# Kernel tuning notes

Measured on AMD Instinct MI355X. Metric: run time of the kernel, lower is better.

The kernel has to match this reference:

```python
import jax, jax.numpy as jnp
import numpy as np

B, S, D = 2, 2048, 1024
H = 16
HD = D // H  # 64
SCALE = HD ** -0.5


def setup_inputs() -> dict:
    key = jax.random.key(0)
    ks = jax.random.split(key, 9)
    init = lambda k, shape: jax.random.normal(k, shape, dtype=jnp.float32) * (1.0 / np.sqrt(shape[-1]))
    return {
        "x": jax.random.normal(ks[0], (B, S, D), dtype=jnp.float32),
        "wq": init(ks[1], (D, D)), "bq": jnp.zeros((D,), jnp.float32),
        "wk": init(ks[2], (D, D)), "bk": jnp.zeros((D,), jnp.float32),
        "wv": init(ks[3], (D, D)), "bv": jnp.zeros((D,), jnp.float32),
        "wo": init(ks[4], (D, D)), "bo": jnp.zeros((D,), jnp.float32),
    }


def reference(x, wq, bq, wk, bk, wv, bv, wo, bo):
    b, s, d = x.shape
    # projections -> [b, h, s, hd]
    q = (x @ wq + bq).reshape(b, s, H, HD).transpose(0, 2, 1, 3)
    k = (x @ wk + bk).reshape(b, s, H, HD).transpose(0, 2, 1, 3)
    v = (x @ wv + bv).reshape(b, s, H, HD).transpose(0, 2, 1, 3)
    # full causal attention (chunked loop in original computes exactly this)
    scores = jnp.einsum("bhqd,bhkd->bhqk", q, k) * SCALE
    causal = jnp.tril(jnp.ones((s, s), dtype=bool))
    scores = jnp.where(causal, scores, -jnp.inf)
    weights = jax.nn.softmax(scores, axis=-1)
    out = jnp.einsum("bhqk,bhkd->bhqd", weights, v)
    out = out.transpose(0, 2, 1, 3).reshape(b, s, d)
    return out @ wo + bo
```

## Files before the change

### kernel.cpp

```cpp
#include <hip/hip_runtime.h>
#include <hip/hip_bf16.h>
#include <cstdint>

#define B_  2
#define S_  2048
#define D_  1024
#define H_  16
#define HD_ 64
#define M_  (B_ * S_)
static constexpr float SC_LOG2E = 0.125f * 1.44269504088896f;

typedef __bf16 bf16x8 __attribute__((ext_vector_type(8)));
typedef __bf16 bf16x4 __attribute__((ext_vector_type(4)));
typedef float  f32x4  __attribute__((ext_vector_type(4)));

#define PPLANE (256 * 2 * 512)

__device__ __forceinline__ unsigned short f2b(float f) {
  union { float f; unsigned u; } x; x.f = f;
  unsigned r = x.u + 0x7FFF + ((x.u >> 16) & 1);
  return (unsigned short)(r >> 16);
}

__device__ __forceinline__ void gl_lds16(const unsigned short* g, unsigned short* l) {
  __builtin_amdgcn_global_load_lds((const __attribute__((address_space(1))) void*)g,
                                   (__attribute__((address_space(3))) void*)l, 16, 0, 0);
}

__device__ __forceinline__ void bar_lgkm() {
  asm volatile("s_waitcnt lgkmcnt(0)\n\ts_barrier" ::: "memory");
}
__device__ __forceinline__ void bar_vm2() {
  asm volatile("s_waitcnt vmcnt(2) lgkmcnt(0)\n\ts_barrier" ::: "memory");
}
__device__ __forceinline__ void bar_vm0() {
  asm volatile("s_waitcnt vmcnt(0) lgkmcnt(0)\n\ts_barrier" ::: "memory");
}

__global__ void cvt_all_kernel(const float* __restrict__ x,
                               const float* __restrict__ w0, const float* __restrict__ w1,
                               const float* __restrict__ w2, const float* __restrict__ w3,
                               unsigned short* __restrict__ xb,
                               unsigned short* __restrict__ o0, unsigned short* __restrict__ o1,
                               unsigned short* __restrict__ o2, unsigned short* __restrict__ o3) {
  int tx = threadIdx.x, ty = threadIdx.y;
  if (blockIdx.z == 4) {
    int tid = ty * 32 + tx;
    int base = ((int)blockIdx.y * 32 + (int)blockIdx.x) * 1024 + tid;
    const float4* xf = (const float4*)x;
    ushort4* ob = (ushort4*)xb;
#pragma unroll
    for (int j = 0; j < 4; j++) {
      float4 v = xf[base + j * 256];
      ushort4 r;
      r.x = f2b(v.x); r.y = f2b(v.y); r.z = f2b(v.z); r.w = f2b(v.w);
      ob[base + j * 256] = r;
    }
    return;
  }
  const float* w = blockIdx.z == 0 ? w0 : blockIdx.z == 1 ? w1 : blockIdx.z == 2 ? w2 : w3;
  unsigned short* o = blockIdx.z == 0 ? o0 : blockIdx.z == 1 ? o1 : blockIdx.z == 2 ? o2 : o3;
  __shared__ float t[32][33];
  int x0 = blockIdx.x * 32, y0 = blockIdx.y * 32;
#pragma unroll
  for (int j = 0; j < 4; j++)
    t[ty + j * 8][tx] = w[(size_t)(y0 + ty + j * 8) * D_ + x0 + tx];
  __syncthreads();
#pragma unroll
  for (int j = 0; j < 4; j++)
    o[(size_t)(x0 + ty + j * 8) * D_ + y0 + tx] = f2b(t[tx][ty + j * 8]);
}

__global__ __launch_bounds__(512) void qkv_gemm_kernel(
    const unsigned short* __restrict__ xb,
    const unsigned short* __restrict__ wqt, const unsigned short* __restrict__ wkt,
    const unsigned short* __restrict__ wvt,
    const float* __restrict__ bq, const float* __restrict__ bk, const float* __restrict__ bv,
    unsigned short* __restrict__ qo, unsigned short* __restrict__ ko, unsigned short* __restrict__ vo) {
  const unsigned short* wt = blockIdx.z == 0 ? wqt : blockIdx.z == 1 ? wkt : wvt;
  const float* bias        = blockIdx.z == 0 ? bq  : blockIdx.z == 1 ? bk  : bv;
  unsigned short* out      = blockIdx.z == 0 ? qo  : blockIdx.z == 1 ? ko  : vo;
  const float scl = blockIdx.z == 0 ? SC_LOG2E : 1.0f;

  __shared__ __align__(16) unsigned short smem[6 * 4096];
  const int tid = threadIdx.x;
  const int lane = tid & 63, wid = tid >> 6;
  const int wm = wid & 1, wn = wid >> 1;
  const int m0 = blockIdx.x * 128, n0 = blockIdx.y * 128;
  const int l15 = lane & 15, q4 = lane >> 4;
  const int srow = tid >> 2, skc = (tid & 3) * 8;

  f32x4 zero = {0.f, 0.f, 0.f, 0.f};
  f32x4 acc[4][2];
#pragma unroll
  for (int mt = 0; mt < 4; mt++)
#pragma unroll
    for (int nt = 0; nt < 2; nt++) acc[mt][nt] = zero;

  const unsigned short* ap = xb + (size_t)(m0 + srow) * D_ + skc;
  const unsigned short* bp = wt + (size_t)(n0 + srow) * D_ + skc;
  gl_lds16(ap,      smem + tid * 8);
  gl_lds16(bp,      smem + 12288 + tid * 8);
  gl_lds16(ap + 32, smem + 4096 + tid * 8);
  gl_lds16(bp + 32, smem + 12288 + 4096 + tid * 8);

  int bc = 0;
  for (int it = 0; it < 32; it++) {
    if (it < 31) bar_vm2(); else bar_vm0();
    if (it + 2 < 32) {
      int bn_ = bc < 1 ? bc + 2 : bc - 1;
      gl_lds16(ap + (it + 2) * 32, smem + bn_ * 4096 + tid * 8);
      gl_lds16(bp + (it + 2) * 32, smem + 12288 + bn_ * 4096 + tid * 8);
    }
    const unsigned short* Ab = smem + bc * 4096;
    const unsigned short* Bb = smem + 12288 + bc * 4096;
    bf16x8 af[4], bfv[2];
#pragma unroll
    for (int mt = 0; mt < 4; mt++) af[mt]  = *(const bf16x8*)(Ab + (wm * 64 + mt * 16 + l15) * 32 + q4 * 8);
#pragma unroll
    for (int nt = 0; nt < 2; nt++) bfv[nt] = *(const bf16x8*)(Bb + (wn * 32 + nt * 16 + l15) * 32 + q4 * 8);
#pragma unroll
    for (int mt = 0; mt < 4; mt++)
#pragma unroll
      for (int nt = 0; nt < 2; nt++)
        acc[mt][nt] = __builtin_amdgcn_mfma_f32_16x16x32_bf16(af[mt], bfv[nt], acc[mt][nt], 0, 0, 0);
    bc = bc == 2 ? 0 : bc + 1;
  }

  if (blockIdx.z < 2) {
#pragma unroll
    for (int nt = 0; nt < 2; nt++) {
      int n = n0 + wn * 32 + nt * 16 + l15;
      float bn = bias[n];
      int h = n >> 6, hd = n & 63;
#pragma unroll
      for (int mt = 0; mt < 4; mt++) {
#pragma unroll
        for (int r = 0; r < 4; r++) {
          int m = m0 + wm * 64 + mt * 16 + q4 * 4 + r;
          int b = m >> 11, s = m & (S_ - 1);
          out[(((size_t)(b * H_ + h)) * S_ + s) * HD_ + hd] = f2b((acc[mt][nt][r] + bn) * scl);
        }
      }
    }
  } else {
    unsigned short* buf = smem;
#pragma unroll
    for (int p = 0; p < 2; p++) {
      __syncthreads();
      if ((wn >> 1) == p) {
#pragma unroll
        for (int nt = 0; nt < 2; nt++) {
          int np = (wn & 1) * 32 + nt * 16 + l15;
          float bn = bias[n0 + p * 64 + np];
#pragma unroll
          for (int mt = 0; mt < 4; mt++) {
            f32x4 vb = acc[mt][nt];
            vb[0] += bn; vb[1] += bn; vb[2] += bn; vb[3] += bn;
            bf16x4 pk = __builtin_convertvector(vb, bf16x4);
            *(bf16x4*)(&buf[np * 136 + wm * 64 + mt * 16 + q4 * 4]) = pk;
          }
        }
      }
      __syncthreads();
#pragma unroll
      for (int i = 0; i < 2; i++) {
        int ci = tid + i * 512;
        int np = ci >> 4, c = ci & 15;
        int n = n0 + p * 64 + np;
        int h = n >> 6, hd = n & 63;
        int m = m0 + c * 8;
        int b = m >> 11, s = m & (S_ - 1);
        *(uint4*)(out + (((size_t)(b * H_ + h)) * HD_ + hd) * S_ + s) = *(const uint4*)(buf + np * 136 + c * 8);
      }
    }
  }
}

__global__ __launch_bounds__(512, 6) void attn_kernel(
    const unsigned short* __restrict__ Q, const unsigned short* __restrict__ K,
    const unsigned short* __restrict__ Vt_g, unsigned short* __restrict__ O,
    float* __restrict__ part) {
  const int id = blockIdx.x;
  const int g = id & 255, r = id >> 8;
  const int bh = g & 31, j = g >> 5;
  const bool heavy = (r < 2);
  const int qi = heavy ? (15 - j) : j;
  const int split = heavy ? r : 0;
  const int b = bh >> 4, h = bh & 15;
  const unsigned short* Qh = Q    + (size_t)bh * S_ * HD_;
  const unsigned short* Kh = K    + (size_t)bh * S_ * HD_;
  const unsigned short* Vh = Vt_g + (size_t)bh * HD_ * S_;

  __shared__ __align__(16) unsigned short Ks[2][64 * 64];
  __shared__ __align__(16) unsigned short Vt[2][64 * 64];
  __shared__ __align__(16) unsigned short Ps[8][16 * 72];

  const int tid = threadIdx.x, lane = tid & 63, w = tid >> 6;
  const int l15 = lane & 15, q4 = lane >> 4;
  const int kx = (l15 & 7) << 3;
  const int kcA = (q4 * 8) ^ kx, kcB = (q4 * 8 + 32) ^ kx;
  const int vc0 = (q4 * 8) ^ kx, vc1 = (32 + q4 * 8) ^ kx;
  unsigned short* Pw = &Ps[w][0];

  const int srow = tid >> 3;
  const int scolS = (((tid & 7) ^ (srow & 7)) * 8);
  const unsigned short* kg = Kh + (size_t)srow * HD_ + (tid & 7) * 8;
  const unsigned short* vg = Vh + (size_t)srow * S_  + (tid & 7) * 8;

  const int q0 = qi * 128;
  const int nst = heavy ? (qi + 1) : (2 * qi + 2);
  const int kstep = heavy ? 2 : 1;
  const int qlo = q0 + w * 16;
  const int qmax = qlo + 15;
  const int qrow = qlo + l15;

  const unsigned short* qp = Qh + (size_t)qrow * HD_ + q4 * 8;
  bf16x8 bq0 = *(const bf16x8*)(qp);
  bf16x8 bq1 = *(const bf16x8*)(qp + 32);

  float m_i = -1e30f, l_i = 0.f;
  f32x4 zero = {0.f, 0.f, 0.f, 0.f};
  f32x4 o_acc[4];
#pragma unroll
  for (int t4 = 0; t4 < 4; t4++) o_acc[t4] = zero;

  uint4 kp = *(const uint4*)(kg + (size_t)split * 64 * HD_);
  uint4 vp = *(const uint4*)(vg + split * 64);

  for (int s = 0; s < nst; s++) {
    const int kt = kstep * s + split;
    const int k0 = kt * 64;
    unsigned short* Kb = Ks[s & 1];
    unsigned short* Vb = Vt[s & 1];
    *(uint4*)(Kb + srow * 64 + scolS) = kp;
    *(uint4*)(Vb + srow * 64 + scolS) = vp;
    bar_lgkm();
    if (s + 1 < nst) {
      const int ktn = kt + kstep;
      kp = *(const uint4*)(kg + (size_t)ktn * 64 * HD_);
      vp = *(const uint4*)(vg + ktn * 64);
    }

    if (k0 <= qmax) {
      f32x4 sc[4];
#pragma unroll
      for (int nt = 0; nt < 4; nt++) sc[nt] = zero;
      __builtin_amdgcn_s_setprio(1);
#pragma unroll
      for (int nt = 0; nt < 4; nt++) {
        bf16x8 ak0 = *(const bf16x8*)(Kb + (nt * 16 + l15) * 64 + kcA);
        bf16x8 ak1 = *(const bf16x8*)(Kb + (nt * 16 + l15) * 64 + kcB);
        sc[nt] = __builtin_amdgcn_mfma_f32_16x16x32_bf16(ak0, bq0, sc[nt], 0, 0, 0);
        sc[nt] = __builtin_amdgcn_mfma_f32_16x16x32_bf16(ak1, bq1, sc[nt], 0, 0, 0);
      }
      __builtin_amdgcn_s_setprio(0);

      if ((k0 + 63) > qlo) {
#pragma unroll
        for (int nt = 0; nt < 4; nt++)
#pragma unroll
          for (int r2 = 0; r2 < 4; r2++) {
            int key = k0 + nt * 16 + q4 * 4 + r2;
            if (key > qrow) sc[nt][r2] = -1e30f;
          }
      }

      float am[4];
#pragma unroll
      for (int nt = 0; nt < 4; nt++)
        am[nt] = fmaxf(fmaxf(sc[nt][0], sc[nt][1]), fmaxf(sc[nt][2], sc[nt][3]));
      am[0] = fmaxf(am[0], am[2]); am[1] = fmaxf(am[1], am[3]);
      float mx = fmaxf(am[0], am[1]);
      mx = fmaxf(mx, __shfl_xor(mx, 16));
      mx = fmaxf(mx, __shfl_xor(mx, 32));
      mx = fmaxf(mx, m_i);

      if (!__all(mx - m_i <= 10.0f)) {
        float alpha = __builtin_amdgcn_exp2f(m_i - mx);
        m_i = mx;
        l_i *= alpha;
#pragma unroll
        for (int r2 = 0; r2 < 4; r2++) {
          float ar = __shfl(alpha, q4 * 4 + r2);
          o_acc[0][r2] *= ar; o_acc[1][r2] *= ar; o_acc[2][r2] *= ar; o_acc[3][r2] *= ar;
        }
      }

      float sm[4];
#pragma unroll
      for (int nt = 0; nt < 4; nt++) {
        f32x4 pv;
#pragma unroll
        for (int r2 = 0; r2 < 4; r2++) pv[r2] = __builtin_amdgcn_exp2f(sc[nt][r2] - m_i);
        sc[nt] = pv;
        sm[nt] = (pv[0] + pv[1]) + (pv[2] + pv[3]);
      }
      float rs = (sm[0] + sm[2]) + (sm[1] + sm[3]);
      rs += __shfl_xor(rs, 16);
      rs += __shfl_xor(rs, 32);
      l_i += rs;

#pragma unroll
      for (int nt = 0; nt < 4; nt++) {
        bf16x4 pk = __builtin_convertvector(sc[nt], bf16x4);
        *(bf16x4*)(Pw + l15 * 72 + nt * 16 + q4 * 4) = pk;
      }
      __threadfence_block();
      bf16x8 ap0 = *(const bf16x8*)(Pw + l15 * 72 + q4 * 8);
      bf16x8 ap1 = *(const bf16x8*)(Pw + l15 * 72 + 32 + q4 * 8);
      __builtin_amdgcn_s_setprio(1);
#pragma unroll
      for (int nt2 = 0; nt2 < 4; nt2++) {
        bf16x8 bv0 = *(const bf16x8*)(Vb + (nt2 * 16 + l15) * 64 + vc0);
        o_acc[nt2] = __builtin_amdgcn_mfma_f32_16x16x32_bf16(ap0, bv0, o_acc[nt2], 0, 0, 0);
      }
#pragma unroll
      for (int nt2 = 0; nt2 < 4; nt2++) {
        bf16x8 bv1 = *(const bf16x8*)(Vb + (nt2 * 16 + l15) * 64 + vc1);
        o_acc[nt2] = __builtin_amdgcn_mfma_f32_16x16x32_bf16(ap1, bv1, o_acc[nt2], 0, 0, 0);
      }
      __builtin_amdgcn_s_setprio(0);
    }
  }

  if (heavy) {
    float* P = part + ((size_t)(g * 2 + split) * 512 + tid);
#pragma unroll
    for (int nt2 = 0; nt2 < 4; nt2++)
#pragma unroll
      for (int r2 = 0; r2 < 4; r2++) P[(size_t)(nt2 * 4 + r2) * PPLANE] = o_acc[nt2][r2];
    P[(size_t)16 * PPLANE] = m_i;
    P[(size_t)17 * PPLANE] = l_i;
  } else {
#pragma unroll
    for (int r2 = 0; r2 < 4; r2++) {
      float lr = __shfl(l_i, q4 * 4 + r2);
      float inv = 1.0f / lr;
      int s_ = q0 + w * 16 + q4 * 4 + r2;
#pragma unroll
      for (int nt2 = 0; nt2 < 4; nt2++)
        O[((size_t)(b * S_ + s_)) * D_ + h * HD_ + nt2 * 16 + l15] = f2b(o_acc[nt2][r2] * inv);
    }
  }
}

__global__ __launch_bounds__(512) void attn_merge_kernel(
    const float* __restrict__ part, unsigned short* __restrict__ O) {
  const int g = blockIdx.x;
  const int bh = g & 31, j = g >> 5;
  const int qi = 15 - j;
  const int b = bh >> 4, h = bh & 15;
  const int tid = threadIdx.x, lane = tid & 63, w = tid >> 6;
  const int l15 = lane & 15, q4 = lane >> 4;

  const float* P0 = part + ((size_t)(g * 2 + 0) * 512 + tid);
  const float* P1 = part + ((size_t)(g * 2 + 1) * 512 + tid);
  float o0[16], o1[16];
#pragma unroll
  for (int i = 0; i < 16; i++) {
    o0[i] = P0[(size_t)i * PPLANE];
    o1[i] = P1[(size_t)i * PPLANE];
  }
  float m0 = P0[(size_t)16 * PPLANE], l0 = P0[(size_t)17 * PPLANE];
  float m1 = P1[(size_t)16 * PPLANE], l1 = P1[(size_t)17 * PPLANE];
  float m  = fmaxf(m0, m1);
  float a0 = __builtin_amdgcn_exp2f(m0 - m);
  float a1 = __builtin_amdgcn_exp2f(m1 - m);
  float l  = l0 * a0 + l1 * a1;

  const int q0 = qi * 128;
#pragma unroll
  for (int r2 = 0; r2 < 4; r2++) {
    float ar0 = __shfl(a0, q4 * 4 + r2);
    float ar1 = __shfl(a1, q4 * 4 + r2);
    float inv = 1.0f / __shfl(l, q4 * 4 + r2);
    int s_ = q0 + w * 16 + q4 * 4 + r2;
#pragma unroll
    for (int nt2 = 0; nt2 < 4; nt2++)
      O[((size_t)(b * S_ + s_)) * D_ + h * HD_ + nt2 * 16 + l15] =
          f2b((o0[nt2 * 4 + r2] * ar0 + o1[nt2 * 4 + r2] * ar1) * inv);
  }
}

__global__ __launch_bounds__(512) void out_gemm_kernel(
    const unsigned short* __restrict__ ab, const unsigned short* __restrict__ wot,
    const float* __restrict__ bo, float* __restrict__ out) {
  __shared__ __align__(16) unsigned short smem[6 * 4096];
  const int tid = threadIdx.x;
  const int lane = tid & 63, wid = tid >> 6;
  const int wm = wid & 1, wn = wid >> 1;
  const int m0 = blockIdx.x * 128, n0 = blockIdx.y * 128;
  const int l15 = lane & 15, q4 = lane >> 4;
  const int srow = tid >> 2, skc = (tid & 3) * 8;

  f32x4 zero = {0.f, 0.f, 0.f, 0.f};
  f32x4 acc[4][2];
#pragma unroll
  for (int mt = 0; mt < 4; mt++)
#pragma unroll
    for (int nt = 0; nt < 2; nt++) acc[mt][nt] = zero;

  const unsigned short* ap = ab  + (size_t)(m0 + srow) * D_ + skc;
  const unsigned short* bp = wot + (size_t)(n0 + srow) * D_ + skc;
  gl_lds16(ap,      smem + tid * 8);
  gl_lds16(bp,      smem + 12288 + tid * 8);
  gl_lds16(ap + 32, smem + 4096 + tid * 8);
  gl_lds16(bp + 32, smem + 12288 + 4096 + tid * 8);

  int bc = 0;
  for (int it = 0; it < 32; it++) {
    if (it < 31) bar_vm2(); else bar_vm0();
    if (it + 2 < 32) {
      int bn_ = bc < 1 ? bc + 2 : bc - 1;
      gl_lds16(ap + (it + 2) * 32, smem + bn_ * 4096 + tid * 8);
      gl_lds16(bp + (it + 2) * 32, smem + 12288 + bn_ * 4096 + tid * 8);
    }
    const unsigned short* Ab = smem + bc * 4096;
    const unsigned short* Bb = smem + 12288 + bc * 4096;
    bf16x8 af[4], bfv[2];
#pragma unroll
    for (int mt = 0; mt < 4; mt++) af[mt]  = *(const bf16x8*)(Ab + (wm * 64 + mt * 16 + l15) * 32 + q4 * 8);
#pragma unroll
    for (int nt = 0; nt < 2; nt++) bfv[nt] = *(const bf16x8*)(Bb + (wn * 32 + nt * 16 + l15) * 32 + q4 * 8);
#pragma unroll
    for (int mt = 0; mt < 4; mt++)
#pragma unroll
      for (int nt = 0; nt < 2; nt++)
        acc[mt][nt] = __builtin_amdgcn_mfma_f32_16x16x32_bf16(af[mt], bfv[nt], acc[mt][nt], 0, 0, 0);
    bc = bc == 2 ? 0 : bc + 1;
  }

#pragma unroll
  for (int nt = 0; nt < 2; nt++) {
    int n = n0 + wn * 32 + nt * 16 + l15;
    float bn = bo[n];
#pragma unroll
    for (int mt = 0; mt < 4; mt++) {
#pragma unroll
      for (int r = 0; r < 4; r++) {
        int m = m0 + wm * 64 + mt * 16 + q4 * 4 + r;
        out[(size_t)m * D_ + n] = acc[mt][nt][r] + bn;
      }
    }
  }
}

extern "C" void kernel_launch(void* const* d_in, const int* in_sizes, int n_in,
                              void* d_out, int out_size, void* d_ws, size_t ws_size,
                              hipStream_t stream) {
  const float* x  = (const float*)d_in[0];
  const float* wq = (const float*)d_in[1];
  const float* bq = (const float*)d_in[2];
  const float* wk = (const float*)d_in[3];
  const float* bk = (const float*)d_in[4];
  const float* wv = (const float*)d_in[5];
  const float* bv = (const float*)d_in[6];
  const float* wo = (const float*)d_in[7];
  const float* bo = (const float*)d_in[8];
  float* out = (float*)d_out;

  char* ws = (char*)d_ws;
  unsigned short* xb  = (unsigned short*)(ws);
  unsigned short* wqt = (unsigned short*)(ws + (8u  << 20));
  unsigned short* wkt = (unsigned short*)(ws + (10u << 20));
  unsigned short* wvt = (unsigned short*)(ws + (12u << 20));
  unsigned short* wot = (unsigned short*)(ws + (14u << 20));
  unsigned short* qb  = (unsigned short*)(ws + (16u << 20));
  unsigned short* kb  = (unsigned short*)(ws + (24u << 20));
  unsigned short* vtg = (unsigned short*)(ws + (32u << 20));
  float*          prt = (float*)(ws + (40u << 20));
  unsigned short* ab  = xb;

  cvt_all_kernel<<<dim3(32, 32, 5), dim3(32, 8), 0, stream>>>(x, wq, wk, wv, wo, xb, wqt, wkt, wvt, wot);
  qkv_gemm_kernel<<<dim3(32, 8, 3), dim3(512), 0, stream>>>(xb, wqt, wkt, wvt, bq, bk, bv, qb, kb, vtg);
  attn_kernel<<<dim3(768), dim3(512), 0, stream>>>(qb, kb, vtg, ab, prt);
  attn_merge_kernel<<<dim3(256), dim3(512), 0, stream>>>(prt, ab);
  out_gemm_kernel<<<dim3(32, 8), dim3(512), 0, stream>>>(ab, wot, bo, out);
}
```

Baseline: 181.5 us.

## Give each attention wave 32 query rows and halve block size to 256 threads

Each wave now processes two 16-row query groups against the same K/V tiles, so the K fragments loaded from LDS are reused across twice as many MFMAs. The block shrinks to 4 waves, each thread stages two K/V chunks, and the partial-result layout and merge kernel are rewritten for the new 256-thread mapping. This roughly doubles accumulator and score registers per wave and lowers the occupancy hint. Causal masking also becomes coarser per wave, which may waste some work on diagonal tiles.

```diff
diff --git a/kernel.cpp b/kernel.cpp
--- a/kernel.cpp
+++ b/kernel.cpp
@@ -14,7 +14,7 @@
 typedef __bf16 bf16x4 __attribute__((ext_vector_type(4)));
 typedef float  f32x4  __attribute__((ext_vector_type(4)));
 
-#define PPLANE (256 * 2 * 512)
+#define PPL2 (256 * 2 * 256)
 
 __device__ __forceinline__ unsigned short f2b(float f) {
   union { float f; unsigned u; } x; x.f = f;
@@ -177,7 +177,7 @@
   }
 }
 
-__global__ __launch_bounds__(512, 6) void attn_kernel(
+__global__ __launch_bounds__(256, 3) void attn_kernel(
     const unsigned short* __restrict__ Q, const unsigned short* __restrict__ K,
     const unsigned short* __restrict__ Vt_g, unsigned short* __restrict__ O,
     float* __restrict__ part) {
@@ -194,7 +194,7 @@
 
   __shared__ __align__(16) unsigned short Ks[2][64 * 64];
   __shared__ __align__(16) unsigned short Vt[2][64 * 64];
-  __shared__ __align__(16) unsigned short Ps[8][16 * 72];
+  __shared__ __align__(16) unsigned short Ps[4][32 * 72];
 
   const int tid = threadIdx.x, lane = tid & 63, w = tid >> 6;
   const int l15 = lane & 15, q4 = lane >> 4;
@@ -203,149 +203,188 @@
   const int vc0 = (q4 * 8) ^ kx, vc1 = (32 + q4 * 8) ^ kx;
   unsigned short* Pw = &Ps[w][0];
 
-  const int srow = tid >> 3;
-  const int scolS = (((tid & 7) ^ (srow & 7)) * 8);
-  const unsigned short* kg = Kh + (size_t)srow * HD_ + (tid & 7) * 8;
-  const unsigned short* vg = Vh + (size_t)srow * S_  + (tid & 7) * 8;
+  int soff[2], kgo[2], vgo[2];
+#pragma unroll
+  for (int jj = 0; jj < 2; jj++) {
+    int c = tid + jj * 256, row = c >> 3, c8 = c & 7;
+    soff[jj] = row * 64 + ((c8 ^ (row & 7)) * 8);
+    kgo[jj] = row * HD_ + c8 * 8;
+    vgo[jj] = row * S_  + c8 * 8;
+  }
 
   const int q0 = qi * 128;
   const int nst = heavy ? (qi + 1) : (2 * qi + 2);
   const int kstep = heavy ? 2 : 1;
-  const int qlo = q0 + w * 16;
-  const int qmax = qlo + 15;
-  const int qrow = qlo + l15;
-
-  const unsigned short* qp = Qh + (size_t)qrow * HD_ + q4 * 8;
-  bf16x8 bq0 = *(const bf16x8*)(qp);
-  bf16x8 bq1 = *(const bf16x8*)(qp + 32);
-
-  float m_i = -1e30f, l_i = 0.f;
+  const int qlo = q0 + w * 32;
+  const int qmax = qlo + 31;
+
+  bf16x8 bq[2][2];
+#pragma unroll
+  for (int grp = 0; grp < 2; grp++) {
+    const unsigned short* qp = Qh + (size_t)(qlo + grp * 16 + l15) * HD_ + q4 * 8;
+    bq[grp][0] = *(const bf16x8*)(qp);
+    bq[grp][1] = *(const bf16x8*)(qp + 32);
+  }
+
+  float m_i[2] = {-1e30f, -1e30f}, l_i[2] = {0.f, 0.f};
   f32x4 zero = {0.f, 0.f, 0.f, 0.f};
-  f32x4 o_acc[4];
-#pragma unroll
-  for (int t4 = 0; t4 < 4; t4++) o_acc[t4] = zero;
-
-  uint4 kp = *(const uint4*)(kg + (size_t)split * 64 * HD_);
-  uint4 vp = *(const uint4*)(vg + split * 64);
+  f32x4 o_acc[2][4];
+#pragma unroll
+  for (int grp = 0; grp < 2; grp++)
+#pragma unroll
+    for (int t4 = 0; t4 < 4; t4++) o_acc[grp][t4] = zero;
+
+  uint4 kp[2], vp[2];
+#pragma unroll
+  for (int jj = 0; jj < 2; jj++) {
+    kp[jj] = *(const uint4*)(Kh + (size_t)split * 64 * HD_ + kgo[jj]);
+    vp[jj] = *(const uint4*)(Vh + split * 64 + vgo[jj]);
+  }
 
   for (int s = 0; s < nst; s++) {
     const int kt = kstep * s + split;
     const int k0 = kt * 64;
     unsigned short* Kb = Ks[s & 1];
     unsigned short* Vb = Vt[s & 1];
-    *(uint4*)(Kb + srow * 64 + scolS) = kp;
-    *(uint4*)(Vb + srow * 64 + scolS) = vp;
+#pragma unroll
+    for (int jj = 0; jj < 2; jj++) {
+      *(uint4*)(Kb + soff[jj]) = kp[jj];
+      *(uint4*)(Vb + soff[jj]) = vp[jj];
+    }
     bar_lgkm();
     if (s + 1 < nst) {
       const int ktn = kt + kstep;
-      kp = *(const uint4*)(kg + (size_t)ktn * 64 * HD_);
-      vp = *(const uint4*)(vg + ktn * 64);
+#pragma unroll
+      for (int jj = 0; jj < 2; jj++) {
+        kp[jj] = *(const uint4*)(Kh + (size_t)ktn * 64 * HD_ + kgo[jj]);
+        vp[jj] = *(const uint4*)(Vh + ktn * 64 + vgo[jj]);
+      }
     }
 
     if (k0 <= qmax) {
-      f32x4 sc[4];
-#pragma unroll
-      for (int nt = 0; nt < 4; nt++) sc[nt] = zero;
+      f32x4 sc[2][4];
+#pragma unroll
+      for (int grp = 0; grp < 2; grp++)
+#pragma unroll
+        for (int nt = 0; nt < 4; nt++) sc[grp][nt] = zero;
       __builtin_amdgcn_s_setprio(1);
 #pragma unroll
       for (int nt = 0; nt < 4; nt++) {
         bf16x8 ak0 = *(const bf16x8*)(Kb + (nt * 16 + l15) * 64 + kcA);
         bf16x8 ak1 = *(const bf16x8*)(Kb + (nt * 16 + l15) * 64 + kcB);
-        sc[nt] = __builtin_amdgcn_mfma_f32_16x16x32_bf16(ak0, bq0, sc[nt], 0, 0, 0);
-        sc[nt] = __builtin_amdgcn_mfma_f32_16x16x32_bf16(ak1, bq1, sc[nt], 0, 0, 0);
+        sc[0][nt] = __builtin_amdgcn_mfma_f32_16x16x32_bf16(ak0, bq[0][0], sc[0][nt], 0, 0, 0);
+        sc[0][nt] = __builtin_amdgcn_mfma_f32_16x16x32_bf16(ak1, bq[0][1], sc[0][nt], 0, 0, 0);
+        sc[1][nt] = __builtin_amdgcn_mfma_f32_16x16x32_bf16(ak0, bq[1][0], sc[1][nt], 0, 0, 0);
+        sc[1][nt] = __builtin_amdgcn_mfma_f32_16x16x32_bf16(ak1, bq[1][1], sc[1][nt], 0, 0, 0);
       }
       __builtin_amdgcn_s_setprio(0);
 
-      if ((k0 + 63) > qlo) {
+#pragma unroll
+      for (int grp = 0; grp < 2; grp++) {
+        const int qg = qlo + grp * 16;
+        const int qrow = qg + l15;
+        if ((k0 + 63) > qg) {
+#pragma unroll
+          for (int nt = 0; nt < 4; nt++)
+#pragma unroll
+            for (int r2 = 0; r2 < 4; r2++) {
+              int key = k0 + nt * 16 + q4 * 4 + r2;
+              if (key > qrow) sc[grp][nt][r2] = -1e30f;
+            }
+        }
+        float am[4];
 #pragma unroll
         for (int nt = 0; nt < 4; nt++)
+          am[nt] = fmaxf(fmaxf(sc[grp][nt][0], sc[grp][nt][1]), fmaxf(sc[grp][nt][2], sc[grp][nt][3]));
+        am[0] = fmaxf(am[0], am[2]); am[1] = fmaxf(am[1], am[3]);
+        float mx = fmaxf(am[0], am[1]);
+        mx = fmaxf(mx, __shfl_xor(mx, 16));
+        mx = fmaxf(mx, __shfl_xor(mx, 32));
+        mx = fmaxf(mx, m_i[grp]);
+
+        if (!__all(mx - m_i[grp] <= 10.0f)) {
+          float alpha = __builtin_amdgcn_exp2f(m_i[grp] - mx);
+          m_i[grp] = mx;
+          l_i[grp] *= alpha;
 #pragma unroll
           for (int r2 = 0; r2 < 4; r2++) {
-            int key = k0 + nt * 16 + q4 * 4 + r2;
-            if (key > qrow) sc[nt][r2] = -1e30f;
+            float ar = __shfl(alpha, q4 * 4 + r2);
+            o_acc[grp][0][r2] *= ar; o_acc[grp][1][r2] *= ar;
+            o_acc[grp][2][r2] *= ar; o_acc[grp][3][r2] *= ar;
           }
-      }
-
-      float am[4];
-#pragma unroll
-      for (int nt = 0; nt < 4; nt++)
-        am[nt] = fmaxf(fmaxf(sc[nt][0], sc[nt][1]), fmaxf(sc[nt][2], sc[nt][3]));
-      am[0] = fmaxf(am[0], am[2]); am[1] = fmaxf(am[1], am[3]);
-      float mx = fmaxf(am[0], am[1]);
-      mx = fmaxf(mx, __shfl_xor(mx, 16));
-      mx = fmaxf(mx, __shfl_xor(mx, 32));
-      mx = fmaxf(mx, m_i);
-
-      if (!__all(mx - m_i <= 10.0f)) {
-        float alpha = __builtin_amdgcn_exp2f(m_i - mx);
-        m_i = mx;
-        l_i *= alpha;
-#pragma unroll
-        for (int r2 = 0; r2 < 4; r2++) {
-          float ar = __shfl(alpha, q4 * 4 + r2);
-          o_acc[0][r2] *= ar; o_acc[1][r2] *= ar; o_acc[2][r2] *= ar; o_acc[3][r2] *= ar;
         }
-      }
-
-      float sm[4];
-#pragma unroll
-      for (int nt = 0; nt < 4; nt++) {
-        f32x4 pv;
-#pragma unroll
-        for (int r2 = 0; r2 < 4; r2++) pv[r2] = __builtin_amdgcn_exp2f(sc[nt][r2] - m_i);
-        sc[nt] = pv;
-        sm[nt] = (pv[0] + pv[1]) + (pv[2] + pv[3]);
-      }
-      float rs = (sm[0] + sm[2]) + (sm[1] + sm[3]);
-      rs += __shfl_xor(rs, 16);
-      rs += __shfl_xor(rs, 32);
-      l_i += rs;
-
-#pragma unroll
-      for (int nt = 0; nt < 4; nt++) {
-        bf16x4 pk = __builtin_convertvector(sc[nt], bf16x4);
-        *(bf16x4*)(Pw + l15 * 72 + nt * 16 + q4 * 4) = pk;
+
+        float sm[4];
+#pragma unroll
+        for (int nt = 0; nt < 4; nt++) {
+          f32x4 pv;
+#pragma unroll
+          for (int r2 = 0; r2 < 4; r2++) pv[r2] = __builtin_amdgcn_exp2f(sc[grp][nt][r2] - m_i[grp]);
+          sc[grp][nt] = pv;
+          sm[nt] = (pv[0] + pv[1]) + (pv[2] + pv[3]);
+        }
+        float rs = (sm[0] + sm[2]) + (sm[1] + sm[3]);
+        rs += __shfl_xor(rs, 16);
+        rs += __shfl_xor(rs, 32);
+        l_i[grp] += rs;
+
+#pragma unroll
+        for (int nt = 0; nt < 4; nt++) {
+          bf16x4 pk = __builtin_convertvector(sc[grp][nt], bf16x4);
+          *(bf16x4*)(Pw + (grp * 16 + l15) * 72 + nt * 16 + q4 * 4) = pk;
+        }
       }
       __threadfence_block();
-      bf16x8 ap0 = *(const bf16x8*)(Pw + l15 * 72 + q4 * 8);
-      bf16x8 ap1 = *(const bf16x8*)(Pw + l15 * 72 + 32 + q4 * 8);
+      bf16x8 a0g0 = *(const bf16x8*)(Pw + l15 * 72 + q4 * 8);
+      bf16x8 a1g0 = *(const bf16x8*)(Pw + l15 * 72 + 32 + q4 * 8);
+      bf16x8 a0g1 = *(const bf16x8*)(Pw + (16 + l15) * 72 + q4 * 8);
+      bf16x8 a1g1 = *(const bf16x8*)(Pw + (16 + l15) * 72 + 32 + q4 * 8);
       __builtin_amdgcn_s_setprio(1);
 #pragma unroll
       for (int nt2 = 0; nt2 < 4; nt2++) {
         bf16x8 bv0 = *(const bf16x8*)(Vb + (nt2 * 16 + l15) * 64 + vc0);
-        o_acc[nt2] = __builtin_amdgcn_mfma_f32_16x16x32_bf16(ap0, bv0, o_acc[nt2], 0, 0, 0);
+        o_acc[0][nt2] = __builtin_amdgcn_mfma_f32_16x16x32_bf16(a0g0, bv0, o_acc[0][nt2], 0, 0, 0);
+        o_acc[1][nt2] = __builtin_amdgcn_mfma_f32_16x16x32_bf16(a0g1, bv0, o_acc[1][nt2], 0, 0, 0);
       }
 #pragma unroll
       for (int nt2 = 0; nt2 < 4; nt2++) {
         bf16x8 bv1 = *(const bf16x8*)(Vb + (nt2 * 16 + l15) * 64 + vc1);
-        o_acc[nt2] = __builtin_amdgcn_mfma_f32_16x16x32_bf16(ap1, bv1, o_acc[nt2], 0, 0, 0);
+        o_acc[0][nt2] = __builtin_amdgcn_mfma_f32_16x16x32_bf16(a1g0, bv1, o_acc[0][nt2], 0, 0, 0);
+        o_acc[1][nt2] = __builtin_amdgcn_mfma_f32_16x16x32_bf16(a1g1, bv1, o_acc[1][nt2], 0, 0, 0);
       }
       __builtin_amdgcn_s_setprio(0);
     }
   }
 
   if (heavy) {
-    float* P = part + ((size_t)(g * 2 + split) * 512 + tid);
-#pragma unroll
-    for (int nt2 = 0; nt2 < 4; nt2++)
-#pragma unroll
-      for (int r2 = 0; r2 < 4; r2++) P[(size_t)(nt2 * 4 + r2) * PPLANE] = o_acc[nt2][r2];
-    P[(size_t)16 * PPLANE] = m_i;
-    P[(size_t)17 * PPLANE] = l_i;
+    float* P = part + ((size_t)(g * 2 + split) * 256 + tid);
+#pragma unroll
+    for (int grp = 0; grp < 2; grp++)
+#pragma unroll
+      for (int nt2 = 0; nt2 < 4; nt2++)
+#pragma unroll
+        for (int r2 = 0; r2 < 4; r2++)
+          P[(size_t)(grp * 16 + nt2 * 4 + r2) * PPL2] = o_acc[grp][nt2][r2];
+    P[(size_t)32 * PPL2] = m_i[0];
+    P[(size_t)33 * PPL2] = m_i[1];
+    P[(size_t)34 * PPL2] = l_i[0];
+    P[(size_t)35 * PPL2] = l_i[1];
   } else {
 #pragma unroll
-    for (int r2 = 0; r2 < 4; r2++) {
-      float lr = __shfl(l_i, q4 * 4 + r2);
-      float inv = 1.0f / lr;
-      int s_ = q0 + w * 16 + q4 * 4 + r2;
-#pragma unroll
-      for (int nt2 = 0; nt2 < 4; nt2++)
-        O[((size_t)(b * S_ + s_)) * D_ + h * HD_ + nt2 * 16 + l15] = f2b(o_acc[nt2][r2] * inv);
-    }
-  }
-}
-
-__global__ __launch_bounds__(512) void attn_merge_kernel(
+    for (int grp = 0; grp < 2; grp++)
+#pragma unroll
+      for (int r2 = 0; r2 < 4; r2++) {
+        float lr = __shfl(l_i[grp], q4 * 4 + r2);
+        float inv = 1.0f / lr;
+        int s_ = qlo + grp * 16 + q4 * 4 + r2;
+#pragma unroll
+        for (int nt2 = 0; nt2 < 4; nt2++)
+          O[((size_t)(b * S_ + s_)) * D_ + h * HD_ + nt2 * 16 + l15] = f2b(o_acc[grp][nt2][r2] * inv);
+      }
+  }
+}
+
+__global__ __launch_bounds__(256) void attn_merge_kernel(
     const float* __restrict__ part, unsigned short* __restrict__ O) {
   const int g = blockIdx.x;
   const int bh = g & 31, j = g >> 5;
@@ -353,33 +392,35 @@
   const int b = bh >> 4, h = bh & 15;
   const int tid = threadIdx.x, lane = tid & 63, w = tid >> 6;
   const int l15 = lane & 15, q4 = lane >> 4;
-
-  const float* P0 = part + ((size_t)(g * 2 + 0) * 512 + tid);
-  const float* P1 = part + ((size_t)(g * 2 + 1) * 512 + tid);
-  float o0[16], o1[16];
-#pragma unroll
-  for (int i = 0; i < 16; i++) {
-    o0[i] = P0[(size_t)i * PPLANE];
-    o1[i] = P1[(size_t)i * PPLANE];
-  }
-  float m0 = P0[(size_t)16 * PPLANE], l0 = P0[(size_t)17 * PPLANE];
-  float m1 = P1[(size_t)16 * PPLANE], l1 = P1[(size_t)17 * PPLANE];
-  float m  = fmaxf(m0, m1);
-  float a0 = __builtin_amdgcn_exp2f(m0 - m);
-  float a1 = __builtin_amdgcn_exp2f(m1 - m);
-  float l  = l0 * a0 + l1 * a1;
-
-  const int q0 = qi * 128;
-#pragma unroll
-  for (int r2 = 0; r2 < 4; r2++) {
-    float ar0 = __shfl(a0, q4 * 4 + r2);
-    float ar1 = __shfl(a1, q4 * 4 + r2);
-    float inv = 1.0f / __shfl(l, q4 * 4 + r2);
-    int s_ = q0 + w * 16 + q4 * 4 + r2;
-#pragma unroll
-    for (int nt2 = 0; nt2 < 4; nt2++)
-      O[((size_t)(b * S_ + s_)) * D_ + h * HD_ + nt2 * 16 + l15] =
-          f2b((o0[nt2 * 4 + r2] * ar0 + o1[nt2 * 4 + r2] * ar1) * inv);
+  const int qlo = qi * 128 + w * 32;
+
+  const float* P0 = part + ((size_t)(g * 2 + 0) * 256 + tid);
+  const float* P1 = part + ((size_t)(g * 2 + 1) * 256 + tid);
+#pragma unroll
+  for (int grp = 0; grp < 2; grp++) {
+    float o0[16], o1[16];
+#pragma unroll
+    for (int i = 0; i < 16; i++) {
+      o0[i] = P0[(size_t)(grp * 16 + i) * PPL2];
+      o1[i] = P1[(size_t)(grp * 16 + i) * PPL2];
+    }
+    float m0 = P0[(size_t)(32 + grp) * PPL2], l0 = P0[(size_t)(34 + grp) * PPL2];
+    float m1 = P1[(size_t)(32 + grp) * PPL2], l1 = P1[(size_t)(34 + grp) * PPL2];
+    float m  = fmaxf(m0, m1);
+    float a0 = __builtin_amdgcn_exp2f(m0 - m);
+    float a1 = __builtin_amdgcn_exp2f(m1 - m);
+    float l  = l0 * a0 + l1 * a1;
+#pragma unroll
+    for (int r2 = 0; r2 < 4; r2++) {
+      float ar0 = __shfl(a0, q4 * 4 + r2);
+      float ar1 = __shfl(a1, q4 * 4 + r2);
+      float inv = 1.0f / __shfl(l, q4 * 4 + r2);
+      int s_ = qlo + grp * 16 + q4 * 4 + r2;
+#pragma unroll
+      for (int nt2 = 0; nt2 < 4; nt2++)
+        O[((size_t)(b * S_ + s_)) * D_ + h * HD_ + nt2 * 16 + l15] =
+            f2b((o0[nt2 * 4 + r2] * ar0 + o1[nt2 * 4 + r2] * ar1) * inv);
+    }
   }
 }
 
@@ -474,7 +515,7 @@
 
   cvt_all_kernel<<<dim3(32, 32, 5), dim3(32, 8), 0, stream>>>(x, wq, wk, wv, wo, xb, wqt, wkt, wvt, wot);
   qkv_gemm_kernel<<<dim3(32, 8, 3), dim3(512), 0, stream>>>(xb, wqt, wkt, wvt, bq, bk, bv, qb, kb, vtg);
-  attn_kernel<<<dim3(768), dim3(512), 0, stream>>>(qb, kb, vtg, ab, prt);
-  attn_merge_kernel<<<dim3(256), dim3(512), 0, stream>>>(prt, ab);
+  attn_kernel<<<dim3(768), dim3(256), 0, stream>>>(qb, kb, vtg, ab, prt);
+  attn_merge_kernel<<<dim3(256), dim3(256), 0, stream>>>(prt, ab);
   out_gemm_kernel<<<dim3(32, 8), dim3(512), 0, stream>>>(ab, wot, bo, out);
 }
```

Result: slower. 199.3 us (+9.8%).

## Fuse split-KV merge into attention via atomic counter, drop merge kernel

Applied to the files above, without the earlier changes.

The separate merge kernel is removed. Each heavy attention block writes its partial output, then increments a per-group atomic counter. The block that arrives second reads the other split's partial from global memory and writes the final normalized output. The counter is zeroed inside the conversion kernel. The P scratch row stride also changes from 72 to 68, which alters LDS bank mapping. This saves one kernel launch and the full re-read of both partials, at the cost of a fence, atomic and extra barriers at the end of heavy blocks.

```diff
diff --git a/kernel.cpp b/kernel.cpp
--- a/kernel.cpp
+++ b/kernel.cpp
@@ -42,10 +42,12 @@
                                const float* __restrict__ w2, const float* __restrict__ w3,
                                unsigned short* __restrict__ xb,
                                unsigned short* __restrict__ o0, unsigned short* __restrict__ o1,
-                               unsigned short* __restrict__ o2, unsigned short* __restrict__ o3) {
+                               unsigned short* __restrict__ o2, unsigned short* __restrict__ o3,
+                               unsigned* __restrict__ ctr) {
   int tx = threadIdx.x, ty = threadIdx.y;
   if (blockIdx.z == 4) {
     int tid = ty * 32 + tx;
+    if (blockIdx.x == 0 && blockIdx.y == 0) ctr[tid] = 0;
     int base = ((int)blockIdx.y * 32 + (int)blockIdx.x) * 1024 + tid;
     const float4* xf = (const float4*)x;
     ushort4* ob = (ushort4*)xb;
@@ -180,7 +182,7 @@
 __global__ __launch_bounds__(512, 6) void attn_kernel(
     const unsigned short* __restrict__ Q, const unsigned short* __restrict__ K,
     const unsigned short* __restrict__ Vt_g, unsigned short* __restrict__ O,
-    float* __restrict__ part) {
+    float* __restrict__ part, unsigned* __restrict__ ctr) {
   const int id = blockIdx.x;
   const int g = id & 255, r = id >> 8;
   const int bh = g & 31, j = g >> 5;
@@ -194,7 +196,8 @@
 
   __shared__ __align__(16) unsigned short Ks[2][64 * 64];
   __shared__ __align__(16) unsigned short Vt[2][64 * 64];
-  __shared__ __align__(16) unsigned short Ps[8][16 * 72];
+  __shared__ __align__(16) unsigned short Ps[8][16 * 68];
+  __shared__ unsigned rendezvous;
 
   const int tid = threadIdx.x, lane = tid & 63, w = tid >> 6;
   const int l15 = lane & 15, q4 = lane >> 4;
@@ -304,11 +307,11 @@
 #pragma unroll
       for (int nt = 0; nt < 4; nt++) {
         bf16x4 pk = __builtin_convertvector(sc[nt], bf16x4);
-        *(bf16x4*)(Pw + l15 * 72 + nt * 16 + q4 * 4) = pk;
+        *(bf16x4*)(Pw + l15 * 68 + nt * 16 + q4 * 4) = pk;
       }
       __threadfence_block();
-      bf16x8 ap0 = *(const bf16x8*)(Pw + l15 * 72 + q4 * 8);
-      bf16x8 ap1 = *(const bf16x8*)(Pw + l15 * 72 + 32 + q4 * 8);
+      bf16x8 ap0 = *(const bf16x8*)(Pw + l15 * 68 + q4 * 8);
+      bf16x8 ap1 = *(const bf16x8*)(Pw + l15 * 68 + 32 + q4 * 8);
       __builtin_amdgcn_s_setprio(1);
 #pragma unroll
       for (int nt2 = 0; nt2 < 4; nt2++) {
@@ -332,6 +335,34 @@
       for (int r2 = 0; r2 < 4; r2++) P[(size_t)(nt2 * 4 + r2) * PPLANE] = o_acc[nt2][r2];
     P[(size_t)16 * PPLANE] = m_i;
     P[(size_t)17 * PPLANE] = l_i;
+
+    __threadfence();
+    __syncthreads();
+    if (tid == 0) rendezvous = atomicAdd(&ctr[g], 1);
+    __syncthreads();
+    if (rendezvous == 1) {
+      __threadfence();
+      const float* Pp = part + ((size_t)(g * 2 + (1 - split)) * 512 + tid);
+      float oo[16];
+#pragma unroll
+      for (int i = 0; i < 16; i++) oo[i] = Pp[(size_t)i * PPLANE];
+      float m1 = Pp[(size_t)16 * PPLANE], l1 = Pp[(size_t)17 * PPLANE];
+      float M  = fmaxf(m_i, m1);
+      float a0 = __builtin_amdgcn_exp2f(m_i - M);
+      float a1 = __builtin_amdgcn_exp2f(m1 - M);
+      float lf = l_i * a0 + l1 * a1;
+#pragma unroll
+      for (int r2 = 0; r2 < 4; r2++) {
+        float ar0 = __shfl(a0, q4 * 4 + r2);
+        float ar1 = __shfl(a1, q4 * 4 + r2);
+        float inv = 1.0f / __shfl(lf, q4 * 4 + r2);
+        int s_ = q0 + w * 16 + q4 * 4 + r2;
+#pragma unroll
+        for (int nt2 = 0; nt2 < 4; nt2++)
+          O[((size_t)(b * S_ + s_)) * D_ + h * HD_ + nt2 * 16 + l15] =
+              f2b((o_acc[nt2][r2] * ar0 + oo[nt2 * 4 + r2] * ar1) * inv);
+      }
+    }
   } else {
 #pragma unroll
     for (int r2 = 0; r2 < 4; r2++) {
@@ -342,44 +373,6 @@
       for (int nt2 = 0; nt2 < 4; nt2++)
         O[((size_t)(b * S_ + s_)) * D_ + h * HD_ + nt2 * 16 + l15] = f2b(o_acc[nt2][r2] * inv);
     }
-  }
-}
-
-__global__ __launch_bounds__(512) void attn_merge_kernel(
-    const float* __restrict__ part, unsigned short* __restrict__ O) {
-  const int g = blockIdx.x;
-  const int bh = g & 31, j = g >> 5;
-  const int qi = 15 - j;
-  const int b = bh >> 4, h = bh & 15;
-  const int tid = threadIdx.x, lane = tid & 63, w = tid >> 6;
-  const int l15 = lane & 15, q4 = lane >> 4;
-
-  const float* P0 = part + ((size_t)(g * 2 + 0) * 512 + tid);
-  const float* P1 = part + ((size_t)(g * 2 + 1) * 512 + tid);
-  float o0[16], o1[16];
-#pragma unroll
-  for (int i = 0; i < 16; i++) {
-    o0[i] = P0[(size_t)i * PPLANE];
-    o1[i] = P1[(size_t)i * PPLANE];
-  }
-  float m0 = P0[(size_t)16 * PPLANE], l0 = P0[(size_t)17 * PPLANE];
-  float m1 = P1[(size_t)16 * PPLANE], l1 = P1[(size_t)17 * PPLANE];
-  float m  = fmaxf(m0, m1);
-  float a0 = __builtin_amdgcn_exp2f(m0 - m);
-  float a1 = __builtin_amdgcn_exp2f(m1 - m);
-  float l  = l0 * a0 + l1 * a1;
-
-  const int q0 = qi * 128;
-#pragma unroll
-  for (int r2 = 0; r2 < 4; r2++) {
-    float ar0 = __shfl(a0, q4 * 4 + r2);
-    float ar1 = __shfl(a1, q4 * 4 + r2);
-    float inv = 1.0f / __shfl(l, q4 * 4 + r2);
-    int s_ = q0 + w * 16 + q4 * 4 + r2;
-#pragma unroll
-    for (int nt2 = 0; nt2 < 4; nt2++)
-      O[((size_t)(b * S_ + s_)) * D_ + h * HD_ + nt2 * 16 + l15] =
-          f2b((o0[nt2 * 4 + r2] * ar0 + o1[nt2 * 4 + r2] * ar1) * inv);
   }
 }
 
@@ -470,11 +463,11 @@
   unsigned short* kb  = (unsigned short*)(ws + (24u << 20));
   unsigned short* vtg = (unsigned short*)(ws + (32u << 20));
   float*          prt = (float*)(ws + (40u << 20));
+  unsigned*       ctr = (unsigned*)(ws + (60u << 20));
   unsigned short* ab  = xb;
 
-  cvt_all_kernel<<<dim3(32, 32, 5), dim3(32, 8), 0, stream>>>(x, wq, wk, wv, wo, xb, wqt, wkt, wvt, wot);
+  cvt_all_kernel<<<dim3(32, 32, 5), dim3(32, 8), 0, stream>>>(x, wq, wk, wv, wo, xb, wqt, wkt, wvt, wot, ctr);
   qkv_gemm_kernel<<<dim3(32, 8, 3), dim3(512), 0, stream>>>(xb, wqt, wkt, wvt, bq, bk, bv, qb, kb, vtg);
-  attn_kernel<<<dim3(768), dim3(512), 0, stream>>>(qb, kb, vtg, ab, prt);
-  attn_merge_kernel<<<dim3(256), dim3(512), 0, stream>>>(prt, ab);
+  attn_kernel<<<dim3(768), dim3(512), 0, stream>>>(qb, kb, vtg, ab, prt, ctr);
   out_gemm_kernel<<<dim3(32, 8), dim3(512), 0, stream>>>(ab, wot, bo, out);
 }
```

Result: slower. 356.6 us (+96.4%).
